# Optimization experiments

Measured on AMD Instinct MI355X. Metric: run time of the kernel, lower is better.

## Reference

```python
import jax, jax.numpy as jnp
import numpy as np

# config
L, N, D, H, I = 4, 16, 64, 1024, 4096   # layers, heads, head_dim, hidden, intermediate
V, P = 50257, 8192                       # vocab, positions
B, S = 2, 2048                           # batch, seq
EPS = 1e-5


def setup_inputs() -> dict:
    key = jax.random.key(0)
    ks = jax.random.split(key, 20)
    std = 0.02
    inp = {
        "input_ids": jax.random.randint(ks[0], (B, S), 0, V),
        "position_ids": jnp.broadcast_to(jnp.arange(S), (B, S)),
        "wte": jax.random.normal(ks[1], (V, H), jnp.float32) * std,
        "wpe": jax.random.normal(ks[2], (P, H), jnp.float32) * std,
        # per-layer stacked params; torch Linear weights are (out, in)
        "ln1_w": jnp.ones((L, H), jnp.float32),
        "ln1_b": jnp.zeros((L, H), jnp.float32),
        "cattn_w": jax.random.normal(ks[3], (L, H + 2 * D, H), jnp.float32) * std,
        "cattn_b": jnp.zeros((L, H + 2 * D), jnp.float32),
        "cproj_w": jax.random.normal(ks[4], (L, H, H), jnp.float32) * std,
        "cproj_b": jnp.zeros((L, H), jnp.float32),
        "ln2_w": jnp.ones((L, H), jnp.float32),
        "ln2_b": jnp.zeros((L, H), jnp.float32),
        "fc_w": jax.random.normal(ks[5], (L, I, H), jnp.float32) * std,
        "fc_b": jnp.zeros((L, I), jnp.float32),
        "mproj_w": jax.random.normal(ks[6], (L, H, I), jnp.float32) * std,
        "mproj_b": jnp.zeros((L, H), jnp.float32),
        "lnf_w": jnp.ones((H,), jnp.float32),
        "lnf_b": jnp.zeros((H,), jnp.float32),
    }
    return inp


def _ln(x, w, b):
    mu = jnp.mean(x, axis=-1, keepdims=True)
    var = jnp.mean(jnp.square(x - mu), axis=-1, keepdims=True)
    return (x - mu) * jax.lax.rsqrt(var + EPS) * w + b


def _forward(input_ids, position_ids, wte, wpe, ln1_w, ln1_b, cattn_w, cattn_b,
             cproj_w, cproj_b, ln2_w, ln2_b, fc_w, fc_b, mproj_w, mproj_b,
             lnf_w, lnf_b):
    h = wte[input_ids] + wpe[position_ids]              # [B,S,H]
    b, s, _ = h.shape
    causal = jnp.tril(jnp.ones((s, s), bool))[None, :, None, :]   # [1,S,1,S] keep-mask
    neg = jnp.finfo(jnp.float32).min
    for l in range(L):
        # --- attention ---
        resid = h
        x = _ln(h, ln1_w[l], ln1_b[l])
        qkv = x @ cattn_w[l].T + cattn_b[l]             # [B,S,H+2D]
        q = qkv[..., :H].reshape(b, s, N, D)
        k = qkv[..., H:H + D]                           # [B,S,D] shared key head
        v = qkv[..., H + D:]                            # [B,S,D] shared value head
        unscale = float(l + 1)
        scale = 1.0 / (unscale * np.sqrt(D))
        scores = jnp.einsum('bsnd,btd->bsnt', q, k) * scale
        # upcast_masked_softmax: to fp32, re-multiply by unscale, mask, softmax
        scores = scores.astype(jnp.float32) * unscale
        scores = jnp.where(causal, scores, neg)
        attn = jax.nn.softmax(scores, axis=-1).astype(h.dtype)
        out = jnp.einsum('bsnt,btd->bsnd', attn, v).reshape(b, s, H)
        h = resid + (out @ cproj_w[l].T + cproj_b[l])
        # --- mlp ---
        resid = h
        x = _ln(h, ln2_w[l], ln2_b[l])
        x = jax.nn.gelu(x @ fc_w[l].T + fc_b[l], approximate=False)
        h = resid + (x @ mproj_w[l].T + mproj_b[l])
    return _ln(h, lnf_w, lnf_b)


def reference(input_ids, position_ids, wte, wpe, ln1_w, ln1_b, cattn_w, cattn_b,
              cproj_w, cproj_b, ln2_w, ln2_b, fc_w, fc_b, mproj_w, mproj_b,
              lnf_w, lnf_b):
    return _forward(input_ids, position_ids, wte, wpe, ln1_w, ln1_b, cattn_w,
                    cattn_b, cproj_w, cproj_b, ln2_w, ln2_b, fc_w, fc_b,
                    mproj_w, mproj_b, lnf_w, lnf_b)
```

## Files before the change

### kernel.cpp

```cpp
#include <hip/hip_runtime.h>
#include <math.h>

typedef __attribute__((ext_vector_type(8))) short short8;
typedef __attribute__((ext_vector_type(8))) __bf16 bf16x8;
typedef __attribute__((ext_vector_type(4))) float f32x4;

static constexpr int H = 1024, LNUM = 4, SEQ = 2048, BATCH = 2;
static constexpr int TOK = BATCH * SEQ;
static constexpr int NI = 4096, QKVD = H + 128;

__device__ __forceinline__ short f2bf(float f) {
  union { float f; unsigned u; } c; c.f = f;
  return (short)((c.u + 0x7fffu + ((c.u >> 16) & 1u)) >> 16);
}

__device__ __forceinline__ void gl_lds16(const short* g, short* l) {
  __builtin_amdgcn_global_load_lds(
      (const __attribute__((address_space(1))) unsigned*)g,
      (__attribute__((address_space(3))) unsigned*)l, 16, 0, 0);
}

#define MFMA16(a, b, c) __builtin_amdgcn_mfma_f32_16x16x32_bf16(a, b, c, 0, 0, 0)

__global__ __launch_bounds__(256) void embed_kernel(
    const int* __restrict__ ids, const int* __restrict__ pos,
    const float* __restrict__ wte, const float* __restrict__ wpe,
    float* __restrict__ h) {
  int i = blockIdx.x * 256 + threadIdx.x;
  int tok = i >> 10, d = i & 1023;
  h[i] = wte[(size_t)ids[tok] * H + d] + wpe[(size_t)pos[tok] * H + d];
}

__global__ __launch_bounds__(256) void cast_kernel(
    const float* __restrict__ src, short* __restrict__ dst) {
  int i = blockIdx.x * 256 + threadIdx.x;
  float4 v = ((const float4*)src)[i];
  union { short s[4]; uint2 u; } p;
  p.s[0] = f2bf(v.x); p.s[1] = f2bf(v.y); p.s[2] = f2bf(v.z); p.s[3] = f2bf(v.w);
  ((uint2*)dst)[i] = p.u;
}

template <bool BF16_OUT>
__global__ __launch_bounds__(256) void ln_kernel(
    const float* __restrict__ X, const float* __restrict__ w,
    const float* __restrict__ b, void* __restrict__ out) {
  int row = blockIdx.x;
  const float* x = X + (size_t)row * H;
  int tid = threadIdx.x, lane = tid & 63, wid = tid >> 6;
  float v[4];
#pragma unroll
  for (int i = 0; i < 4; i++) v[i] = x[tid + i * 256];
  float s = v[0] + v[1] + v[2] + v[3];
#pragma unroll
  for (int off = 32; off > 0; off >>= 1) s += __shfl_xor(s, off);
  __shared__ float red[8];
  if (lane == 0) red[wid] = s;
  __syncthreads();
  float mu = (red[0] + red[1] + red[2] + red[3]) * (1.0f / H);
  float q = 0.f;
#pragma unroll
  for (int i = 0; i < 4; i++) { float d = v[i] - mu; q += d * d; }
#pragma unroll
  for (int off = 32; off > 0; off >>= 1) q += __shfl_xor(q, off);
  if (lane == 0) red[4 + wid] = q;
  __syncthreads();
  float var = (red[4] + red[5] + red[6] + red[7]) * (1.0f / H);
  float inv = rsqrtf(var + 1e-5f);
#pragma unroll
  for (int i = 0; i < 4; i++) {
    int col = tid + i * 256;
    float r = (v[i] - mu) * inv * w[col] + b[col];
    if (BF16_OUT) ((short*)out)[(size_t)row * H + col] = f2bf(r);
    else          ((float*)out)[(size_t)row * H + col] = r;
  }
}

template <int MODE>
__global__ __launch_bounds__(256) void gemm_mfma(
    const short* __restrict__ A, const short* __restrict__ W,
    const float* __restrict__ bias, void* __restrict__ Cv,
    int M, int N, int K) {
  __shared__ short As[128 * 32];
  __shared__ short Bs[128 * 32];
  int tid = threadIdx.x, wave = tid >> 6, lane = tid & 63;
  int li = lane & 15, lg = lane >> 4;
  int row0 = blockIdx.y * 128, col0 = blockIdx.x * 128;
  int wm = (wave & 1) * 64, wn = (wave >> 1) * 64;
  f32x4 acc[4][4] = {};
  const short* Ab = A + (size_t)(row0 + (tid >> 2)) * K + (tid & 3) * 8;
  const short* Wb = W + (size_t)(col0 + (tid >> 2)) * K + (tid & 3) * 8;
  for (int k0 = 0; k0 < K; k0 += 32) {
    __syncthreads();
    gl_lds16(Ab + k0,            As + tid * 8);
    gl_lds16(Ab + k0 + 64 * K,   As + 2048 + tid * 8);
    gl_lds16(Wb + k0,            Bs + tid * 8);
    gl_lds16(Wb + k0 + 64 * K,   Bs + 2048 + tid * 8);
    __syncthreads();
    bf16x8 af[4], bfr[4];
#pragma unroll
    for (int i = 0; i < 4; ++i) {
      af[i]  = *(const bf16x8*)&As[(wm + i * 16 + li) * 32 + lg * 8];
      bfr[i] = *(const bf16x8*)&Bs[(wn + i * 16 + li) * 32 + lg * 8];
    }
#pragma unroll
    for (int i = 0; i < 4; ++i)
#pragma unroll
      for (int j = 0; j < 4; ++j) acc[i][j] = MFMA16(af[i], bfr[j], acc[i][j]);
  }
  float* Cf = (float*)Cv;
  short* Cs = (short*)Cv;
#pragma unroll
  for (int i = 0; i < 4; ++i) {
    int gr = row0 + wm + i * 16 + lg * 4;
#pragma unroll
    for (int j = 0; j < 4; ++j) {
      int gc = col0 + wn + j * 16 + li;
      float bv = bias[gc];
#pragma unroll
      for (int r = 0; r < 4; ++r) {
        float v = acc[i][j][r] + bv;
        size_t idx = (size_t)(gr + r) * N + gc;
        if (MODE == 1) {
          Cf[idx] += v;
        } else if (MODE == 2) {
          v = 0.5f * v * (1.0f + erff(v * 0.70710678118654752f));
          Cs[idx] = f2bf(v);
        } else {
          Cs[idx] = f2bf(v);
        }
      }
    }
  }
}

__global__ __launch_bounds__(256) void mqa_attn(
    const short* __restrict__ qkv, short* __restrict__ out) {
  int head = blockIdx.x, qt = blockIdx.y, b = blockIdx.z;
  int tid = threadIdx.x, wave = tid >> 6, lane = tid & 63;
  int li = lane & 15, lg = lane >> 4;

  __shared__ short Kc[64 * 72];
  __shared__ short VT[64 * 72];
  __shared__ short Ps[4 * 16 * 72];

  const size_t qrow0 = (size_t)(b * SEQ + qt * 64);
  bf16x8 qf[2];
  {
    const short* qp = qkv + (qrow0 + wave * 16 + li) * QKVD + head * 64 + lg * 8;
    qf[0] = *(const bf16x8*)(qp);
    qf[1] = *(const bf16x8*)(qp + 32);
  }
  f32x4 oacc[4] = {};
  float m_i[4], l_i[4];
#pragma unroll
  for (int r = 0; r < 4; ++r) { m_i[r] = -1e30f; l_i[r] = 0.f; }

  int t_ = tid >> 3, c_ = tid & 7;
  for (int j = 0; j <= qt; ++j) {
    __syncthreads();
    {
      const short* g0 = qkv + ((size_t)(b * SEQ + j * 64 + t_)) * QKVD;
      const short* g1 = g0 + 32 * QKVD;
      short8 k0 = *(const short8*)(g0 + 1024 + c_ * 8);
      short8 k1 = *(const short8*)(g1 + 1024 + c_ * 8);
      short8 v0 = *(const short8*)(g0 + 1088 + c_ * 8);
      short8 v1 = *(const short8*)(g1 + 1088 + c_ * 8);
      *(short8*)&Kc[t_ * 72 + c_ * 8] = k0;
      *(short8*)&Kc[(t_ + 32) * 72 + c_ * 8] = k1;
#pragma unroll
      for (int e = 0; e < 8; ++e) {
        VT[(c_ * 8 + e) * 72 + t_] = v0[e];
        VT[(c_ * 8 + e) * 72 + t_ + 32] = v1[e];
      }
    }
    __syncthreads();

    f32x4 s[4];
#pragma unroll
    for (int n = 0; n < 4; ++n) {
      bf16x8 kf0 = *(const bf16x8*)&Kc[(n * 16 + li) * 72 + lg * 8];
      bf16x8 kf1 = *(const bf16x8*)&Kc[(n * 16 + li) * 72 + 32 + lg * 8];
      f32x4 a = {};
      a = MFMA16(qf[0], kf0, a);
      a = MFMA16(qf[1], kf1, a);
      s[n] = a;
    }
    bool diag = (j == qt);
#pragma unroll
    for (int n = 0; n < 4; ++n)
#pragma unroll
      for (int r = 0; r < 4; ++r) {
        float v = s[n][r] * 0.125f;
        if (diag && (n * 16 + li) > (wave * 16 + lg * 4 + r)) v = -1e30f;
        s[n][r] = v;
      }
    float alpha[4];
#pragma unroll
    for (int r = 0; r < 4; ++r) {
      float mx = fmaxf(fmaxf(s[0][r], s[1][r]), fmaxf(s[2][r], s[3][r]));
#pragma unroll
      for (int off = 1; off < 16; off <<= 1) mx = fmaxf(mx, __shfl_xor(mx, off));
      float mn = fmaxf(m_i[r], mx);
      alpha[r] = __expf(m_i[r] - mn);
      m_i[r] = mn;
      float ps = 0.f;
#pragma unroll
      for (int n = 0; n < 4; ++n) {
        float p = __expf(s[n][r] - mn);
        s[n][r] = p;
        ps += p;
      }
#pragma unroll
      for (int off = 1; off < 16; off <<= 1) ps += __shfl_xor(ps, off);
      l_i[r] = l_i[r] * alpha[r] + ps;
    }
#pragma unroll
    for (int dn = 0; dn < 4; ++dn)
#pragma unroll
      for (int r = 0; r < 4; ++r) oacc[dn][r] *= alpha[r];
    short* pw = Ps + wave * 1152;
#pragma unroll
    for (int n = 0; n < 4; ++n)
#pragma unroll
      for (int r = 0; r < 4; ++r) pw[(lg * 4 + r) * 72 + n * 16 + li] = f2bf(s[n][r]);
#pragma unroll
    for (int ks = 0; ks < 2; ++ks) {
      bf16x8 pf = *(const bf16x8*)&pw[li * 72 + ks * 32 + lg * 8];
#pragma unroll
      for (int dn = 0; dn < 4; ++dn) {
        bf16x8 vf = *(const bf16x8*)&VT[(dn * 16 + li) * 72 + ks * 32 + lg * 8];
        oacc[dn] = MFMA16(pf, vf, oacc[dn]);
      }
    }
  }
#pragma unroll
  for (int r = 0; r < 4; ++r) {
    float inv = 1.0f / l_i[r];
    size_t row = (qrow0 + wave * 16 + lg * 4 + r) * H + head * 64;
#pragma unroll
    for (int dn = 0; dn < 4; ++dn) out[row + dn * 16 + li] = f2bf(oacc[dn][r] * inv);
  }
}

extern "C" void kernel_launch(void* const* d_in, const int* in_sizes, int n_in,
                              void* d_out, int out_size, void* d_ws, size_t ws_size,
                              hipStream_t stream) {
  const int*   input_ids    = (const int*)d_in[0];
  const int*   position_ids = (const int*)d_in[1];
  const float* wte     = (const float*)d_in[2];
  const float* wpe     = (const float*)d_in[3];
  const float* ln1_w   = (const float*)d_in[4];
  const float* ln1_b   = (const float*)d_in[5];
  const float* cattn_w = (const float*)d_in[6];
  const float* cattn_b = (const float*)d_in[7];
  const float* cproj_w = (const float*)d_in[8];
  const float* cproj_b = (const float*)d_in[9];
  const float* ln2_w   = (const float*)d_in[10];
  const float* ln2_b   = (const float*)d_in[11];
  const float* fc_w    = (const float*)d_in[12];
  const float* fc_b    = (const float*)d_in[13];
  const float* mproj_w = (const float*)d_in[14];
  const float* mproj_b = (const float*)d_in[15];
  const float* lnf_w   = (const float*)d_in[16];
  const float* lnf_b   = (const float*)d_in[17];

  float* h     = (float*)d_ws;
  short* xbf   = (short*)(h + (size_t)TOK * H);
  short* qkvbf = xbf + (size_t)TOK * H;
  short* fcbf  = qkvbf + (size_t)TOK * QKVD;
  short* wqkv  = fcbf + (size_t)TOK * NI;
  short* wcp   = wqkv + (size_t)QKVD * H;
  short* wfc   = wcp + (size_t)H * H;
  short* wmp   = wfc + (size_t)NI * H;

  embed_kernel<<<TOK * H / 256, 256, 0, stream>>>(input_ids, position_ids, wte, wpe, h);

  for (int l = 0; l < LNUM; l++) {
    cast_kernel<<<QKVD * H / 1024, 256, 0, stream>>>(cattn_w + (size_t)l * QKVD * H, wqkv);
    cast_kernel<<<H * H / 1024, 256, 0, stream>>>(cproj_w + (size_t)l * H * H, wcp);
    cast_kernel<<<NI * H / 1024, 256, 0, stream>>>(fc_w + (size_t)l * NI * H, wfc);
    cast_kernel<<<H * NI / 1024, 256, 0, stream>>>(mproj_w + (size_t)l * H * NI, wmp);

    ln_kernel<true><<<TOK, 256, 0, stream>>>(h, ln1_w + l * H, ln1_b + l * H, xbf);
    gemm_mfma<0><<<dim3(QKVD / 128, TOK / 128), 256, 0, stream>>>(
        xbf, wqkv, cattn_b + (size_t)l * QKVD, qkvbf, TOK, QKVD, H);
    mqa_attn<<<dim3(16, 32, BATCH), 256, 0, stream>>>(qkvbf, xbf);
    gemm_mfma<1><<<dim3(H / 128, TOK / 128), 256, 0, stream>>>(
        xbf, wcp, cproj_b + (size_t)l * H, h, TOK, H, H);
    ln_kernel<true><<<TOK, 256, 0, stream>>>(h, ln2_w + l * H, ln2_b + l * H, xbf);
    gemm_mfma<2><<<dim3(NI / 128, TOK / 128), 256, 0, stream>>>(
        xbf, wfc, fc_b + (size_t)l * NI, fcbf, TOK, NI, H);
    gemm_mfma<1><<<dim3(H / 128, TOK / 128), 256, 0, stream>>>(
        fcbf, wmp, mproj_b + (size_t)l * H, h, TOK, H, NI);
  }
  ln_kernel<false><<<TOK, 256, 0, stream>>>(h, lnf_w, lnf_b, d_out);
}
```

Baseline: 1.962 ms.

## Pretranspose V globally, compute S transposed, keep P in registers via bpermute

Adds a kernel that transposes the shared V head into a global [B,64,SEQ] buffer, so attention can load V with vector stores instead of scalar transposed LDS writes. The QK MFMA swaps operands so each lane owns one query row, which cuts the softmax reductions to two cross-lane shuffles. P is packed to bf16 with v_cvt_pk_bf16_f32 and redistributed with ds_bpermute instead of a round trip through shared memory. Query tiles are reordered to interleave long and short causal tiles for load balance. The cost is an extra kernel launch, reuse of the fc buffer as scratch, and more intricate lane mapping that risks correctness errors.

New measurement: 1.834 ms. 6.5% less time.

```diff
diff --git a/kernel.cpp b/kernel.cpp
--- a/kernel.cpp
+++ b/kernel.cpp
@@ -18,6 +18,12 @@
   __builtin_amdgcn_global_load_lds(
       (const __attribute__((address_space(1))) unsigned*)g,
       (__attribute__((address_space(3))) unsigned*)l, 16, 0, 0);
+}
+
+__device__ __forceinline__ unsigned cvtpk_bf16(float lo, float hi) {
+  unsigned r;
+  asm("v_cvt_pk_bf16_f32 %0, %1, %2" : "=v"(r) : "v"(lo), "v"(hi));
+  return r;
 }
 
 #define MFMA16(a, b, c) __builtin_amdgcn_mfma_f32_16x16x32_bf16(a, b, c, 0, 0, 0)
@@ -133,15 +139,30 @@
   }
 }
 
+__global__ __launch_bounds__(256) void vtrans_kernel(
+    const short* __restrict__ qkv, short* __restrict__ vt) {
+  int i = blockIdx.x * 256 + threadIdx.x;
+  int d  = i & 63;
+  int tc = (i >> 6) & 255;
+  int b  = i >> 14;
+  const short* src = qkv + ((size_t)(b * SEQ + tc * 8)) * QKVD + 1088 + d;
+  short8 v;
+#pragma unroll
+  for (int e = 0; e < 8; ++e) v[e] = src[(size_t)e * QKVD];
+  *(short8*)(vt + ((size_t)(b * 64 + d)) * SEQ + tc * 8) = v;
+}
+
 __global__ __launch_bounds__(256) void mqa_attn(
-    const short* __restrict__ qkv, short* __restrict__ out) {
-  int head = blockIdx.x, qt = blockIdx.y, b = blockIdx.z;
+    const short* __restrict__ qkv, const short* __restrict__ vtg,
+    short* __restrict__ out) {
+  int head = blockIdx.y, b = blockIdx.z;
+  int s = (blockIdx.x + head * 8) & 31;
+  int qt = (s & 1) ? (31 - (s >> 1)) : (s >> 1);
   int tid = threadIdx.x, wave = tid >> 6, lane = tid & 63;
   int li = lane & 15, lg = lane >> 4;
 
   __shared__ short Kc[64 * 72];
-  __shared__ short VT[64 * 72];
-  __shared__ short Ps[4 * 16 * 72];
+  __shared__ short Vt[64 * 72];
 
   const size_t qrow0 = (size_t)(b * SEQ + qt * 64);
   bf16x8 qf[2];
@@ -151,91 +172,101 @@
     qf[1] = *(const bf16x8*)(qp + 32);
   }
   f32x4 oacc[4] = {};
-  float m_i[4], l_i[4];
-#pragma unroll
-  for (int r = 0; r < 4; ++r) { m_i[r] = -1e30f; l_i[r] = 0.f; }
+  float m_i = -1e30f, l_i = 0.f;
 
   int t_ = tid >> 3, c_ = tid & 7;
+  const short* kg = qkv + (size_t)(b * SEQ) * QKVD + 1024;
+  const short* vg = vtg + (size_t)(b * 64 + t_) * SEQ;
+
   for (int j = 0; j <= qt; ++j) {
     __syncthreads();
     {
-      const short* g0 = qkv + ((size_t)(b * SEQ + j * 64 + t_)) * QKVD;
-      const short* g1 = g0 + 32 * QKVD;
-      short8 k0 = *(const short8*)(g0 + 1024 + c_ * 8);
-      short8 k1 = *(const short8*)(g1 + 1024 + c_ * 8);
-      short8 v0 = *(const short8*)(g0 + 1088 + c_ * 8);
-      short8 v1 = *(const short8*)(g1 + 1088 + c_ * 8);
+      const short* g0 = kg + (size_t)(j * 64 + t_) * QKVD + c_ * 8;
+      short8 k0 = *(const short8*)(g0);
+      short8 k1 = *(const short8*)(g0 + 32 * QKVD);
+      short8 v0 = *(const short8*)(vg + j * 64 + c_ * 8);
+      short8 v1 = *(const short8*)(vg + 32 * SEQ + j * 64 + c_ * 8);
       *(short8*)&Kc[t_ * 72 + c_ * 8] = k0;
       *(short8*)&Kc[(t_ + 32) * 72 + c_ * 8] = k1;
-#pragma unroll
-      for (int e = 0; e < 8; ++e) {
-        VT[(c_ * 8 + e) * 72 + t_] = v0[e];
-        VT[(c_ * 8 + e) * 72 + t_ + 32] = v1[e];
-      }
+      *(short8*)&Vt[t_ * 72 + c_ * 8] = v0;
+      *(short8*)&Vt[(t_ + 32) * 72 + c_ * 8] = v1;
     }
     __syncthreads();
 
-    f32x4 s[4];
+    f32x4 s4[4];
 #pragma unroll
     for (int n = 0; n < 4; ++n) {
       bf16x8 kf0 = *(const bf16x8*)&Kc[(n * 16 + li) * 72 + lg * 8];
       bf16x8 kf1 = *(const bf16x8*)&Kc[(n * 16 + li) * 72 + 32 + lg * 8];
       f32x4 a = {};
-      a = MFMA16(qf[0], kf0, a);
-      a = MFMA16(qf[1], kf1, a);
-      s[n] = a;
+      a = MFMA16(kf0, qf[0], a);
+      a = MFMA16(kf1, qf[1], a);
+      s4[n] = a;
     }
     bool diag = (j == qt);
+    float p[4][4];
 #pragma unroll
     for (int n = 0; n < 4; ++n)
 #pragma unroll
       for (int r = 0; r < 4; ++r) {
-        float v = s[n][r] * 0.125f;
-        if (diag && (n * 16 + li) > (wave * 16 + lg * 4 + r)) v = -1e30f;
-        s[n][r] = v;
+        float v = s4[n][r] * 0.125f;
+        if (diag && (n * 16 + lg * 4 + r) > (wave * 16 + li)) v = -1e30f;
+        p[n][r] = v;
       }
-    float alpha[4];
-#pragma unroll
-    for (int r = 0; r < 4; ++r) {
-      float mx = fmaxf(fmaxf(s[0][r], s[1][r]), fmaxf(s[2][r], s[3][r]));
-#pragma unroll
-      for (int off = 1; off < 16; off <<= 1) mx = fmaxf(mx, __shfl_xor(mx, off));
-      float mn = fmaxf(m_i[r], mx);
-      alpha[r] = __expf(m_i[r] - mn);
-      m_i[r] = mn;
-      float ps = 0.f;
-#pragma unroll
-      for (int n = 0; n < 4; ++n) {
-        float p = __expf(s[n][r] - mn);
-        s[n][r] = p;
-        ps += p;
+    float mx = p[0][0];
+#pragma unroll
+    for (int n = 0; n < 4; ++n)
+#pragma unroll
+      for (int r = 0; r < 4; ++r) mx = fmaxf(mx, p[n][r]);
+    mx = fmaxf(mx, __shfl_xor(mx, 16));
+    mx = fmaxf(mx, __shfl_xor(mx, 32));
+    float mn = fmaxf(m_i, mx);
+    float alpha = __expf(m_i - mn);
+    m_i = mn;
+    float ps = 0.f;
+#pragma unroll
+    for (int n = 0; n < 4; ++n)
+#pragma unroll
+      for (int r = 0; r < 4; ++r) { float e = __expf(p[n][r] - mn); p[n][r] = e; ps += e; }
+    ps += __shfl_xor(ps, 16);
+    ps += __shfl_xor(ps, 32);
+    l_i = l_i * alpha + ps;
+    float arow[4];
+#pragma unroll
+    for (int r = 0; r < 4; ++r) arow[r] = __shfl(alpha, (lane >> 4) * 20 + r);
+#pragma unroll
+    for (int dn = 0; dn < 4; ++dn)
+#pragma unroll
+      for (int r = 0; r < 4; ++r) oacc[dn][r] *= arow[r];
+    unsigned pk[4][2];
+#pragma unroll
+    for (int n = 0; n < 4; ++n) {
+      pk[n][0] = cvtpk_bf16(p[n][0], p[n][1]);
+      pk[n][1] = cvtpk_bf16(p[n][2], p[n][3]);
+    }
+#pragma unroll
+    for (int ks = 0; ks < 2; ++ks) {
+      union { unsigned w[4]; bf16x8 v; } pu;
+#pragma unroll
+      for (int d = 0; d < 4; ++d) {
+        int sl = (li + ((lg & 1) << 5) + ((d >> 1) << 4)) << 2;
+        unsigned a0 = __builtin_amdgcn_ds_bpermute(sl, (int)pk[2 * ks][d & 1]);
+        unsigned a1 = __builtin_amdgcn_ds_bpermute(sl, (int)pk[2 * ks + 1][d & 1]);
+        pu.w[d] = (lg >> 1) ? a1 : a0;
       }
 #pragma unroll
-      for (int off = 1; off < 16; off <<= 1) ps += __shfl_xor(ps, off);
-      l_i[r] = l_i[r] * alpha[r] + ps;
-    }
-#pragma unroll
-    for (int dn = 0; dn < 4; ++dn)
-#pragma unroll
-      for (int r = 0; r < 4; ++r) oacc[dn][r] *= alpha[r];
-    short* pw = Ps + wave * 1152;
-#pragma unroll
-    for (int n = 0; n < 4; ++n)
-#pragma unroll
-      for (int r = 0; r < 4; ++r) pw[(lg * 4 + r) * 72 + n * 16 + li] = f2bf(s[n][r]);
-#pragma unroll
-    for (int ks = 0; ks < 2; ++ks) {
-      bf16x8 pf = *(const bf16x8*)&pw[li * 72 + ks * 32 + lg * 8];
-#pragma unroll
       for (int dn = 0; dn < 4; ++dn) {
-        bf16x8 vf = *(const bf16x8*)&VT[(dn * 16 + li) * 72 + ks * 32 + lg * 8];
-        oacc[dn] = MFMA16(pf, vf, oacc[dn]);
+        bf16x8 vf = *(const bf16x8*)&Vt[(dn * 16 + li) * 72 + ks * 32 + lg * 8];
+        oacc[dn] = MFMA16(pu.v, vf, oacc[dn]);
       }
     }
   }
+  float lrow[4];
+#pragma unroll
+  for (int r = 0; r < 4; ++r) lrow[r] = __shfl(l_i, (lane >> 4) * 20 + r);
 #pragma unroll
   for (int r = 0; r < 4; ++r) {
-    float inv = 1.0f / l_i[r];
+    float inv = 1.0f / lrow[r];
     size_t row = (qrow0 + wave * 16 + lg * 4 + r) * H + head * 64;
 #pragma unroll
     for (int dn = 0; dn < 4; ++dn) out[row + dn * 16 + li] = f2bf(oacc[dn][r] * inv);
@@ -272,6 +303,7 @@
   short* wcp   = wqkv + (size_t)QKVD * H;
   short* wfc   = wcp + (size_t)H * H;
   short* wmp   = wfc + (size_t)NI * H;
+  short* vtg   = fcbf;
 
   embed_kernel<<<TOK * H / 256, 256, 0, stream>>>(input_ids, position_ids, wte, wpe, h);
 
@@ -284,7 +316,8 @@
     ln_kernel<true><<<TOK, 256, 0, stream>>>(h, ln1_w + l * H, ln1_b + l * H, xbf);
     gemm_mfma<0><<<dim3(QKVD / 128, TOK / 128), 256, 0, stream>>>(
         xbf, wqkv, cattn_b + (size_t)l * QKVD, qkvbf, TOK, QKVD, H);
-    mqa_attn<<<dim3(16, 32, BATCH), 256, 0, stream>>>(qkvbf, xbf);
+    vtrans_kernel<<<(2 * 64 * SEQ / 8) / 256, 256, 0, stream>>>(qkvbf, vtg);
+    mqa_attn<<<dim3(32, 16, BATCH), 256, 0, stream>>>(qkvbf, vtg, xbf);
     gemm_mfma<1><<<dim3(H / 128, TOK / 128), 256, 0, stream>>>(
         xbf, wcp, cproj_b + (size_t)l * H, h, TOK, H, H);
     ln_kernel<true><<<TOK, 256, 0, stream>>>(h, ln2_w + l * H, ln2_b + l * H, xbf);
```
